# Kernel tuning notes

Hardware: AMD Instinct MI355X
Metric: run time of the kernel (lower is better)

The kernel has to match this reference:

```python
import jax, jax.numpy as jnp
import numpy as np

INPUT_DIM = 1024
OUTPUT_DIM = 1024
SPLINE_POINTS = 4

def setup_inputs() -> dict:
    key = jax.random.key(0)
    k1, k2 = jax.random.split(key)
    x = jax.random.normal(k1, (4096, INPUT_DIM), dtype=jnp.float32)
    spline_coeffs = jax.random.normal(k2, (OUTPUT_DIM, INPUT_DIM, SPLINE_POINTS, 4), dtype=jnp.float32)
    return {"x": x, "spline_coeffs": spline_coeffs}

def reference(x, spline_coeffs):
    # Per-feature min-max normalization over the batch dim (as in the torch code,
    # where x[:, j].min()/max() are taken over the batch).
    xmin = jnp.min(x, axis=0, keepdims=True)   # [1, D]
    xmax = jnp.max(x, axis=0, keepdims=True)
    xn = (x - xmin) / (xmax - xmin)            # [B, D]

    # The original sums the cubic polynomial over all spline_points, so the
    # effective coefficients are the sum over the spline_points axis.
    c = jnp.sum(spline_coeffs, axis=2)         # [O, D, 4]

    x2 = xn * xn
    x3 = x2 * xn
    # out[b, o] = sum_d c0*x^3 + c1*x^2 + c2*x + c3
    out = (jnp.einsum('bd,od->bo', x3, c[..., 0])
           + jnp.einsum('bd,od->bo', x2, c[..., 1])
           + jnp.einsum('bd,od->bo', xn, c[..., 2])
           + jnp.sum(c[..., 3], axis=1)[None, :])
    return out
```

## Files before the change

### kernel.cpp

```cpp
#include <hip/hip_runtime.h>
#include <hip/hip_bf16.h>
#include <stdint.h>
#include <stddef.h>

typedef __bf16 bf16;
typedef __attribute__((ext_vector_type(4))) __bf16 bf16x4;
typedef __attribute__((ext_vector_type(8))) __bf16 bf16x8;
typedef __attribute__((ext_vector_type(4))) float f32x4;

#define BATCH 4096
#define DIM 1024
#define ODIM 1024
#define K3 3072

#define WS_CB     0
#define WS_BIAS   6291456
#define WS_PMIN   6295552
#define WS_PMAX   7344128
#define WS_MINV   8392704
#define WS_SCALE  8396800

#define BARRIER()                     \
  do {                                \
    asm volatile("" ::: "memory");    \
    __builtin_amdgcn_s_barrier();     \
    asm volatile("" ::: "memory");    \
  } while (0)
#define WAIT_LGKM() __builtin_amdgcn_s_waitcnt(0xC07F)

__global__ void k_stream(const float* __restrict__ x,
                         float* __restrict__ pmin,
                         float* __restrict__ pmax,
                         const float* __restrict__ sp,
                         bf16* __restrict__ CB,
                         float* __restrict__ bias) {
  __shared__ float red[4];
  const int t = threadIdx.x;
  if (blockIdx.x < 256) {
    const int ch = blockIdx.x;
    const float* p = x + (size_t)ch * 16 * DIM + (t << 2);
    f32x4 mn = {1e30f, 1e30f, 1e30f, 1e30f};
    f32x4 mx = {-1e30f, -1e30f, -1e30f, -1e30f};
#pragma unroll
    for (int r = 0; r < 16; ++r) {
      f32x4 v = *(const f32x4*)(p + (size_t)r * DIM);
#pragma unroll
      for (int j = 0; j < 4; ++j) {
        mn[j] = fminf(mn[j], v[j]);
        mx[j] = fmaxf(mx[j], v[j]);
      }
    }
    *(f32x4*)(pmin + ch * DIM + (t << 2)) = mn;
    *(f32x4*)(pmax + ch * DIM + (t << 2)) = mx;
  } else {
    const int o = blockIdx.x - 256;
    const int d = t << 2;
    f32x4 s[4];
#pragma unroll
    for (int dd = 0; dd < 4; ++dd) {
      const float* p = sp + ((size_t)o * DIM + d + dd) * 16;
      f32x4 acc = *(const f32x4*)(p);
      acc += *(const f32x4*)(p + 4);
      acc += *(const f32x4*)(p + 8);
      acc += *(const f32x4*)(p + 12);
      s[dd] = acc;
    }
    size_t cb = (size_t)o * K3 + d;
    bf16x4 c0 = {(bf16)s[0][0], (bf16)s[1][0], (bf16)s[2][0], (bf16)s[3][0]};
    bf16x4 c1 = {(bf16)s[0][1], (bf16)s[1][1], (bf16)s[2][1], (bf16)s[3][1]};
    bf16x4 c2 = {(bf16)s[0][2], (bf16)s[1][2], (bf16)s[2][2], (bf16)s[3][2]};
    *(bf16x4*)(CB + cb) = c0;
    *(bf16x4*)(CB + cb + 1024) = c1;
    *(bf16x4*)(CB + cb + 2048) = c2;
    float v = s[0][3] + s[1][3] + s[2][3] + s[3][3];
#pragma unroll
    for (int off = 32; off > 0; off >>= 1) v += __shfl_down(v, off, 64);
    int lane = t & 63, w = t >> 6;
    if (lane == 0) red[w] = v;
    __syncthreads();
    if (t == 0) bias[o] = red[0] + red[1] + red[2] + red[3];
  }
}

__global__ void k_minmax_final(const float* __restrict__ pmin,
                               const float* __restrict__ pmax,
                               float* __restrict__ minv,
                               float* __restrict__ scale) {
  __shared__ float smn[4][64], smx[4][64];
  const int t = threadIdx.x;
  const int lane = t & 63;
  const int w = t >> 6;
  const int col = blockIdx.x * 64 + lane;
  float mn = 1e30f, mx = -1e30f;
#pragma unroll 8
  for (int ch = w; ch < 256; ch += 4) {
    mn = fminf(mn, pmin[ch * DIM + col]);
    mx = fmaxf(mx, pmax[ch * DIM + col]);
  }
  smn[w][lane] = mn;
  smx[w][lane] = mx;
  __syncthreads();
  if (w == 0) {
    mn = fminf(fminf(smn[0][lane], smn[1][lane]), fminf(smn[2][lane], smn[3][lane]));
    mx = fmaxf(fmaxf(smx[0][lane], smx[1][lane]), fmaxf(smx[2][lane], smx[3][lane]));
    minv[col] = mn;
    scale[col] = 1.0f / (mx - mn);
  }
}

#define MSOFF 98304
#define ABUF(b) ((b) * 49152)
__global__ __launch_bounds__(512, 2) void k_gemm(const float* __restrict__ x,
                                                 const float* __restrict__ minv,
                                                 const float* __restrict__ scale,
                                                 const bf16* __restrict__ CBm,
                                                 const float* __restrict__ bias,
                                                 float* __restrict__ out) {
  __shared__ __attribute__((aligned(16))) char smem[106496];

  const int tid = threadIdx.x;
  const int wave = tid >> 6;
  const int lane = tid & 63;

  const int f = blockIdx.x;
  const int chunk = f & 7;
  const int idx = f >> 3;
  const int mt = ((chunk >> 1) << 3) + (idx >> 2);
  const int nt = ((chunk & 1) << 2) + (idx & 3);
  const int bm = mt * 128;
  const int bn = nt * 128;

  const int wr = (wave >> 2) * 64;
  const int wc = (wave & 3) * 32;
  const int mrow = lane & 15;
  const int kq = lane >> 4;

  const int prow = tid >> 2;
  const int cq = tid & 3;
  const int c0 = cq << 4;
  const int s0 = (((cq << 1)) ^ (prow & 7)) << 4;
  const int s1 = (((cq << 1) | 1) ^ (prow & 7)) << 4;

  const float* xg = x + (size_t)(bm + prow) * DIM + c0;

  if (tid < 256) {
    f32x4 m = *(const f32x4*)(minv + tid * 4);
    *(f32x4*)(smem + MSOFF + tid * 16) = m;
  } else {
    f32x4 s = *(const f32x4*)(scale + (tid - 256) * 4);
    *(f32x4*)(smem + MSOFF + 4096 + (tid - 256) * 16) = s;
  }

  f32x4 xv0, xv1, xv2, xv3;
#define LOADX(dtv)                                                            \
  do {                                                                        \
    const float* xp_ = xg + (dtv) * 64;                                       \
    xv0 = *(const f32x4*)(xp_);                                               \
    xv1 = *(const f32x4*)(xp_ + 4);                                           \
    xv2 = *(const f32x4*)(xp_ + 8);                                           \
    xv3 = *(const f32x4*)(xp_ + 12);                                          \
  } while (0)

#define POWERS_WRITE(abuf, dtv)                                               \
  do {                                                                        \
    const char* ms_ = smem + MSOFF + ((dtv) * 64 + c0) * 4;                   \
    f32x4 xn0 = (xv0 - *(const f32x4*)(ms_)) * *(const f32x4*)(ms_ + 4096);   \
    f32x4 xn1 = (xv1 - *(const f32x4*)(ms_ + 16)) * *(const f32x4*)(ms_ + 4112); \
    f32x4 xn2 = (xv2 - *(const f32x4*)(ms_ + 32)) * *(const f32x4*)(ms_ + 4128); \
    f32x4 xn3 = (xv3 - *(const f32x4*)(ms_ + 48)) * *(const f32x4*)(ms_ + 4144); \
    f32x4 x20 = xn0 * xn0, x21 = xn1 * xn1, x22 = xn2 * xn2, x23 = xn3 * xn3; \
    f32x4 x30 = x20 * xn0, x31 = x21 * xn1, x32 = x22 * xn2, x33 = x23 * xn3; \
    bf16x8 w3lo, w3hi, w2lo, w2hi, w1lo, w1hi;                                \
    _Pragma("unroll") for (int e = 0; e < 4; ++e) {                           \
      w3lo[e] = (bf16)x30[e]; w3lo[e + 4] = (bf16)x31[e];                     \
      w3hi[e] = (bf16)x32[e]; w3hi[e + 4] = (bf16)x33[e];                     \
      w2lo[e] = (bf16)x20[e]; w2lo[e + 4] = (bf16)x21[e];                     \
      w2hi[e] = (bf16)x22[e]; w2hi[e + 4] = (bf16)x23[e];                     \
      w1lo[e] = (bf16)xn0[e]; w1lo[e + 4] = (bf16)xn1[e];                     \
      w1hi[e] = (bf16)xn2[e]; w1hi[e + 4] = (bf16)xn3[e];                     \
    }                                                                         \
    char* aw_ = smem + ABUF(abuf) + prow * 128;                               \
    *(bf16x8*)(aw_ + s0) = w3lo;                                              \
    *(bf16x8*)(aw_ + s1) = w3hi;                                              \
    *(bf16x8*)(aw_ + 16384 + s0) = w2lo;                                      \
    *(bf16x8*)(aw_ + 16384 + s1) = w2hi;                                      \
    *(bf16x8*)(aw_ + 32768 + s0) = w1lo;                                      \
    *(bf16x8*)(aw_ + 32768 + s1) = w1hi;                                      \
  } while (0)

  f32x4 acc[4][2] = {};
  const char* cbT = (const char*)CBm + (size_t)(bn + wc + mrow) * 6144 + kq * 16;

#define COMPUTE(abuf, dtv)                                                    \
  do {                                                                        \
    _Pragma("unroll") for (int p = 0; p < 3; ++p) {                           \
      const char* cb_ = cbT + p * 2048 + (dtv) * 128;                         \
      bf16x8 bg[2][2];                                                        \
      _Pragma("unroll") for (int j = 0; j < 2; ++j)                           \
        _Pragma("unroll") for (int ks = 0; ks < 2; ++ks)                      \
            bg[j][ks] = *(const bf16x8*)(cb_ + (size_t)j * 16 * 6144 + ks * 64); \
      const char* ab_ = smem + ABUF(abuf) + p * 16384;                        \
      _Pragma("unroll") for (int ks = 0; ks < 2; ++ks) {                      \
        bf16x8 af[4];                                                         \
        _Pragma("unroll") for (int i = 0; i < 4; ++i) {                       \
          int row_ = wr + i * 16 + mrow;                                      \
          int su_ = ((ks * 4 + kq) ^ (row_ & 7)) * 16;                        \
          af[i] = *(const bf16x8*)(ab_ + row_ * 128 + su_);                   \
        }                                                                     \
        _Pragma("unroll") for (int i = 0; i < 4; ++i)                         \
            _Pragma("unroll") for (int j = 0; j < 2; ++j)                     \
                acc[i][j] = __builtin_amdgcn_mfma_f32_16x16x32_bf16(          \
                    af[i], bg[j][ks], acc[i][j], 0, 0, 0);                    \
      }                                                                       \
    }                                                                         \
  } while (0)

  LOADX(0);
  WAIT_LGKM();
  BARRIER();
  POWERS_WRITE(0, 0);
  LOADX(1);
  WAIT_LGKM();
  BARRIER();

#pragma unroll 2
  for (int dt = 0; dt < 15; ++dt) {
    COMPUTE(dt & 1, dt);
    POWERS_WRITE((dt + 1) & 1, dt + 1);
    if (dt < 14) LOADX(dt + 2);
    WAIT_LGKM();
    BARRIER();
  }
  COMPUTE(1, 15);

  const int ccol = lane & 15;
  const int crow = (lane >> 4) * 4;
#pragma unroll
  for (int j = 0; j < 2; ++j) {
    const int col = bn + wc + j * 16 + ccol;
    const float bv = bias[col];
#pragma unroll
    for (int i = 0; i < 4; ++i) {
      const int row0 = bm + wr + i * 16 + crow;
#pragma unroll
      for (int r = 0; r < 4; ++r)
        out[(size_t)(row0 + r) * ODIM + col] = acc[i][j][r] + bv;
    }
  }
#undef LOADX
#undef POWERS_WRITE
#undef COMPUTE
}

extern "C" void kernel_launch(void* const* d_in, const int* in_sizes, int n_in,
                              void* d_out, int out_size, void* d_ws, size_t ws_size,
                              hipStream_t stream) {
  (void)in_sizes; (void)n_in; (void)out_size; (void)ws_size;
  const float* x = (const float*)d_in[0];
  const float* sp = (const float*)d_in[1];
  float* out = (float*)d_out;
  char* ws = (char*)d_ws;

  bf16* CBm = (bf16*)(ws + WS_CB);
  float* bias = (float*)(ws + WS_BIAS);
  float* pmin = (float*)(ws + WS_PMIN);
  float* pmax = (float*)(ws + WS_PMAX);
  float* minv = (float*)(ws + WS_MINV);
  float* scale = (float*)(ws + WS_SCALE);

  k_stream<<<1280, 256, 0, stream>>>(x, pmin, pmax, sp, CBm, bias);
  k_minmax_final<<<16, 256, 0, stream>>>(pmin, pmax, minv, scale);
  k_gemm<<<256, 512, 0, stream>>>(x, minv, scale, CBm, bias, out);
}
```

Measured before the change: 173.7 us.

## Stage B tiles into LDS via async global_load_lds with halved K-step

The GEMM kernel now stages the weight (B) tiles into shared memory with asynchronous global-to-LDS loads, double-buffered alongside the A powers buffer, instead of each wave reading B fragments directly from global memory. The K step per iteration is halved from 64 to 32 columns so both A and B buffers fit in LDS, which doubles the loop trip count and the barrier count. This aims to cut redundant global reads of B across waves and to overlap B fetches with MFMA work. The cost is a full vmcnt wait every iteration and more barriers per tile.

```diff
diff --git a/kernel.cpp b/kernel.cpp
--- a/kernel.cpp
+++ b/kernel.cpp
@@ -20,12 +20,18 @@
 #define WS_MINV   8392704
 #define WS_SCALE  8396800
 
+#define ASYNC16(g, l)                                                          \
+  __builtin_amdgcn_global_load_lds(                                            \
+      (__attribute__((address_space(1))) void*)(g),                            \
+      (__attribute__((address_space(3))) void*)(l), 16, 0, 0)
+
 #define BARRIER()                     \
   do {                                \
     asm volatile("" ::: "memory");    \
     __builtin_amdgcn_s_barrier();     \
     asm volatile("" ::: "memory");    \
   } while (0)
+#define WAIT_VM0() __builtin_amdgcn_s_waitcnt(0x0F00 | 0x0070)
 #define WAIT_LGKM() __builtin_amdgcn_s_waitcnt(0xC07F)
 
 __global__ void k_stream(const float* __restrict__ x,
@@ -109,7 +115,8 @@
 }
 
 #define MSOFF 98304
-#define ABUF(b) ((b) * 49152)
+#define ABUF(b) ((b) * 24576)
+#define BBUF(b) (49152 + (b) * 24576)
 __global__ __launch_bounds__(512, 2) void k_gemm(const float* __restrict__ x,
                                                  const float* __restrict__ minv,
                                                  const float* __restrict__ scale,
@@ -136,12 +143,12 @@
   const int kq = lane >> 4;
 
   const int prow = tid >> 2;
-  const int cq = tid & 3;
-  const int c0 = cq << 4;
-  const int s0 = (((cq << 1)) ^ (prow & 7)) << 4;
-  const int s1 = (((cq << 1) | 1) ^ (prow & 7)) << 4;
-
-  const float* xg = x + (size_t)(bm + prow) * DIM + c0;
+  const int u = tid & 3;
+  const int aslot = (u ^ ((prow >> 1) & 3)) << 4;
+  const float* xg = x + (size_t)(bm + prow) * DIM + u * 8;
+
+  const char* gBp = (const char*)CBm + (size_t)(bn + (tid >> 2)) * 6144 +
+                    (size_t)(((tid & 3) ^ ((tid >> 3) & 3)) << 4);
 
   if (tid < 256) {
     f32x4 m = *(const f32x4*)(minv + tid * 4);
@@ -151,71 +158,73 @@
     *(f32x4*)(smem + MSOFF + 4096 + (tid - 256) * 16) = s;
   }
 
-  f32x4 xv0, xv1, xv2, xv3;
+  f32x4 xa, xb;
 #define LOADX(dtv)                                                            \
   do {                                                                        \
-    const float* xp_ = xg + (dtv) * 64;                                       \
-    xv0 = *(const f32x4*)(xp_);                                               \
-    xv1 = *(const f32x4*)(xp_ + 4);                                           \
-    xv2 = *(const f32x4*)(xp_ + 8);                                           \
-    xv3 = *(const f32x4*)(xp_ + 12);                                          \
+    xa = *(const f32x4*)(xg + (dtv) * 32);                                    \
+    xb = *(const f32x4*)(xg + (dtv) * 32 + 4);                                \
+  } while (0)
+
+#define STAGE_B(buf, dtv)                                                     \
+  do {                                                                        \
+    const char* gb_ = gBp + (size_t)(dtv) * 64;                               \
+    char* lb_ = smem + BBUF(buf) + wave * 1024;                               \
+    ASYNC16(gb_, lb_);                                                        \
+    ASYNC16(gb_ + 2048, lb_ + 8192);                                          \
+    ASYNC16(gb_ + 4096, lb_ + 16384);                                         \
   } while (0)
 
 #define POWERS_WRITE(abuf, dtv)                                               \
   do {                                                                        \
-    const char* ms_ = smem + MSOFF + ((dtv) * 64 + c0) * 4;                   \
-    f32x4 xn0 = (xv0 - *(const f32x4*)(ms_)) * *(const f32x4*)(ms_ + 4096);   \
-    f32x4 xn1 = (xv1 - *(const f32x4*)(ms_ + 16)) * *(const f32x4*)(ms_ + 4112); \
-    f32x4 xn2 = (xv2 - *(const f32x4*)(ms_ + 32)) * *(const f32x4*)(ms_ + 4128); \
-    f32x4 xn3 = (xv3 - *(const f32x4*)(ms_ + 48)) * *(const f32x4*)(ms_ + 4144); \
-    f32x4 x20 = xn0 * xn0, x21 = xn1 * xn1, x22 = xn2 * xn2, x23 = xn3 * xn3; \
-    f32x4 x30 = x20 * xn0, x31 = x21 * xn1, x32 = x22 * xn2, x33 = x23 * xn3; \
-    bf16x8 w3lo, w3hi, w2lo, w2hi, w1lo, w1hi;                                \
+    const char* msp = smem + MSOFF + ((dtv) * 32 + u * 8) * 4;                \
+    f32x4 mn0 = *(const f32x4*)(msp);                                         \
+    f32x4 mn1 = *(const f32x4*)(msp + 16);                                    \
+    f32x4 sc0 = *(const f32x4*)(msp + 4096);                                  \
+    f32x4 sc1 = *(const f32x4*)(msp + 4112);                                  \
+    f32x4 n0 = (xa - mn0) * sc0, n1 = (xb - mn1) * sc1;                       \
+    f32x4 q0 = n0 * n0, q1 = n1 * n1;                                         \
+    f32x4 c0v = q0 * n0, c1v = q1 * n1;                                       \
+    bf16x8 w1, w2, w3;                                                        \
     _Pragma("unroll") for (int e = 0; e < 4; ++e) {                           \
-      w3lo[e] = (bf16)x30[e]; w3lo[e + 4] = (bf16)x31[e];                     \
-      w3hi[e] = (bf16)x32[e]; w3hi[e + 4] = (bf16)x33[e];                     \
-      w2lo[e] = (bf16)x20[e]; w2lo[e + 4] = (bf16)x21[e];                     \
-      w2hi[e] = (bf16)x22[e]; w2hi[e + 4] = (bf16)x23[e];                     \
-      w1lo[e] = (bf16)xn0[e]; w1lo[e + 4] = (bf16)xn1[e];                     \
-      w1hi[e] = (bf16)xn2[e]; w1hi[e + 4] = (bf16)xn3[e];                     \
+      w3[e] = (bf16)c0v[e]; w3[e + 4] = (bf16)c1v[e];                         \
+      w2[e] = (bf16)q0[e];  w2[e + 4] = (bf16)q1[e];                          \
+      w1[e] = (bf16)n0[e];  w1[e + 4] = (bf16)n1[e];                          \
     }                                                                         \
-    char* aw_ = smem + ABUF(abuf) + prow * 128;                               \
-    *(bf16x8*)(aw_ + s0) = w3lo;                                              \
-    *(bf16x8*)(aw_ + s1) = w3hi;                                              \
-    *(bf16x8*)(aw_ + 16384 + s0) = w2lo;                                      \
-    *(bf16x8*)(aw_ + 16384 + s1) = w2hi;                                      \
-    *(bf16x8*)(aw_ + 32768 + s0) = w1lo;                                      \
-    *(bf16x8*)(aw_ + 32768 + s1) = w1hi;                                      \
+    char* aw_ = smem + ABUF(abuf) + prow * 64 + aslot;                        \
+    *(bf16x8*)(aw_) = w3;                                   \
+    *(bf16x8*)(aw_ + 8192) = w2;                            \
+    *(bf16x8*)(aw_ + 16384) = w1;                           \
   } while (0)
 
   f32x4 acc[4][2] = {};
-  const char* cbT = (const char*)CBm + (size_t)(bn + wc + mrow) * 6144 + kq * 16;
-
-#define COMPUTE(abuf, dtv)                                                    \
-  do {                                                                        \
+
+#define COMPUTE(buf)                                                          \
+  do {                                                                        \
+    const char* ab_ = smem + ABUF(buf);                                       \
+    const char* bb_ = smem + BBUF(buf);                                       \
     _Pragma("unroll") for (int p = 0; p < 3; ++p) {                           \
-      const char* cb_ = cbT + p * 2048 + (dtv) * 128;                         \
-      bf16x8 bg[2][2];                                                        \
-      _Pragma("unroll") for (int j = 0; j < 2; ++j)                           \
-        _Pragma("unroll") for (int ks = 0; ks < 2; ++ks)                      \
-            bg[j][ks] = *(const bf16x8*)(cb_ + (size_t)j * 16 * 6144 + ks * 64); \
-      const char* ab_ = smem + ABUF(abuf) + p * 16384;                        \
-      _Pragma("unroll") for (int ks = 0; ks < 2; ++ks) {                      \
-        bf16x8 af[4];                                                         \
-        _Pragma("unroll") for (int i = 0; i < 4; ++i) {                       \
-          int row_ = wr + i * 16 + mrow;                                      \
-          int su_ = ((ks * 4 + kq) ^ (row_ & 7)) * 16;                        \
-          af[i] = *(const bf16x8*)(ab_ + row_ * 128 + su_);                   \
-        }                                                                     \
-        _Pragma("unroll") for (int i = 0; i < 4; ++i)                         \
-            _Pragma("unroll") for (int j = 0; j < 2; ++j)                     \
-                acc[i][j] = __builtin_amdgcn_mfma_f32_16x16x32_bf16(          \
-                    af[i], bg[j][ks], acc[i][j], 0, 0, 0);                    \
+      bf16x8 bg[2];                                                           \
+      _Pragma("unroll") for (int j = 0; j < 2; ++j) {                         \
+        int rowb = wc + j * 16 + mrow;                                        \
+        bg[j] = *(const bf16x8*)(bb_ + p * 8192 + rowb * 64 +                 \
+                                 ((kq ^ ((rowb >> 1) & 3)) << 4));            \
       }                                                                       \
+      bf16x8 af[4];                                                           \
+      _Pragma("unroll") for (int i = 0; i < 4; ++i) {                         \
+        int rowa = wr + i * 16 + mrow;                                        \
+        af[i] = *(const bf16x8*)(ab_ + p * 8192 + rowa * 64 +                 \
+                                 ((kq ^ ((rowa >> 1) & 3)) << 4));            \
+      }                                                                       \
+      _Pragma("unroll") for (int i = 0; i < 4; ++i)                           \
+          _Pragma("unroll") for (int j = 0; j < 2; ++j)                       \
+              acc[i][j] = __builtin_amdgcn_mfma_f32_16x16x32_bf16(            \
+                  af[i], bg[j], acc[i][j], 0, 0, 0);                          \
     }                                                                         \
   } while (0)
 
+  STAGE_B(0, 0);
   LOADX(0);
+  WAIT_VM0();
   WAIT_LGKM();
   BARRIER();
   POWERS_WRITE(0, 0);
@@ -224,14 +233,15 @@
   BARRIER();
 
 #pragma unroll 2
-  for (int dt = 0; dt < 15; ++dt) {
-    COMPUTE(dt & 1, dt);
-    POWERS_WRITE((dt + 1) & 1, dt + 1);
-    if (dt < 14) LOADX(dt + 2);
+  for (int dt = 0; dt < 32; ++dt) {
+    if (dt < 31) STAGE_B((dt + 1) & 1, dt + 1);
+    COMPUTE(dt & 1);
+    if (dt < 31) POWERS_WRITE((dt + 1) & 1, dt + 1);
+    WAIT_VM0();
+    if (dt < 30) LOADX(dt + 2);
     WAIT_LGKM();
     BARRIER();
   }
-  COMPUTE(1, 15);
 
   const int ccol = lane & 15;
   const int crow = (lane >> 4) * 4;
@@ -248,6 +258,7 @@
     }
   }
 #undef LOADX
+#undef STAGE_B
 #undef POWERS_WRITE
 #undef COMPUTE
 }
```

Measured after the change: 151.1 us, median of 2. -13.0%, faster.
